# Optimization experiments

Hardware: AMD Instinct MI355X
Metric: run time of the kernel (lower is better)

The kernel has to match this reference:

```python
import jax, jax.numpy as jnp
import numpy as np

N, A, C = 4, 8732, 81
SCALE_XY, SCALE_WH = 0.1, 0.2   # dboxes.scale_xy / scale_wh; Loss uses reciprocals
LAM, W_IOU = 1.0, 0.01
EPS_IOU = float(np.finfo(float).eps)


def setup_inputs() -> dict:
    key = jax.random.key(0)
    ks = jax.random.split(key, 8)
    ploc = jax.random.normal(ks[0], (N, 4, A), dtype=jnp.float32) * 0.5
    plabel = jax.random.normal(ks[1], (N, C, A), dtype=jnp.float32)
    # ground-truth loc in xywh with strictly positive wh (loc_vec takes a log)
    gxy = jax.random.uniform(ks[2], (N, 2, A), dtype=jnp.float32)
    gwh = jax.random.uniform(ks[3], (N, 2, A), dtype=jnp.float32) * 0.4 + 0.05
    gloc = jnp.concatenate([gxy, gwh], axis=1)
    lab = jax.random.randint(ks[4], (N, A), 1, C)
    keep = jax.random.uniform(ks[5], (N, A)) < 0.02
    glabel = jnp.where(keep, lab, 0).astype(jnp.int32)
    # default boxes in xywh, shape [1, 4, A]
    dxy = jax.random.uniform(ks[6], (1, 2, A), dtype=jnp.float32)
    dwh = jax.random.uniform(ks[7], (1, 2, A), dtype=jnp.float32) * 0.45 + 0.05
    dboxes = jnp.concatenate([dxy, dwh], axis=1)
    return {"ploc": ploc, "plabel": plabel, "gloc": gloc, "glabel": glabel, "dboxes": dboxes}


def _decode_ltrb(loc, dboxes):
    """scale_back_batch: encoded [N,4,A] + dboxes xywh [1,4,A] -> ltrb [N,A,4]."""
    b = jnp.transpose(loc, (0, 2, 1))      # [N, A, 4]
    d = jnp.transpose(dboxes, (0, 2, 1))   # [1, A, 4]
    xy = SCALE_XY * b[..., :2] * d[..., 2:] + d[..., :2]
    wh = jnp.exp(SCALE_WH * b[..., 2:]) * d[..., 2:]
    return jnp.concatenate([xy - 0.5 * wh, xy + 0.5 * wh], axis=-1)


def _iou_sum(p, g):
    """p, g: [A,4] ltrb -> per-anchor sum over all g boxes of IoU(p_i, g_k)."""
    area_p = (p[:, 2] - p[:, 0]) * (p[:, 3] - p[:, 1])
    area_g = (g[:, 2] - g[:, 0]) * (g[:, 3] - g[:, 1])
    iw = jnp.maximum(jnp.minimum(p[:, None, 2], g[None, :, 2]) - jnp.maximum(p[:, None, 0], g[None, :, 0]), 0.0)
    ih = jnp.maximum(jnp.minimum(p[:, None, 3], g[None, :, 3]) - jnp.maximum(p[:, None, 1], g[None, :, 1]), 0.0)
    inter = iw * ih                                      # [A, A]
    ua = jnp.maximum(area_p[:, None] + area_g[None, :] - inter, EPS_IOU)
    return (inter / ua).sum(axis=1)                      # [A]


def _forward(ploc, plabel, gloc, glabel, dboxes):
    mask = glabel > 0                                    # [N, A]
    pos_num = mask.sum(axis=1)                           # [N]

    # loc_vec: encode ground truth against default boxes
    dxy, dwh = dboxes[:, :2, :], dboxes[:, 2:, :]
    gxy_t = (1.0 / SCALE_XY) * (gloc[:, :2, :] - dxy) / dwh
    gwh_t = (1.0 / SCALE_WH) * jnp.log(gloc[:, 2:, :] / dwh)
    vec_gd = jnp.concatenate([gxy_t, gwh_t], axis=1)     # [N, 4, A]

    # SmoothL1 (beta=1), summed over coord dim
    diff = ploc - vec_gd
    ad = jnp.abs(diff)
    sl1 = jnp.where(ad < 1.0, 0.5 * diff * diff, ad - 0.5).sum(axis=1)  # [N, A]

    # per-anchor cross entropy
    logp = jax.nn.log_softmax(plabel, axis=1)            # [N, C, A]
    con = -jnp.take_along_axis(logp, glabel[:, None, :], axis=1)[:, 0, :]  # [N, A]

    # weighted-IoU reweighting (weights are detached in the original)
    p_ltrb = _decode_ltrb(ploc, dboxes)                  # [N, A, 4]
    g_ltrb = _decode_ltrb(gloc, dboxes)
    iou_s = jax.vmap(_iou_sum)(p_ltrb, g_ltrb)           # [N, A]
    valid = (p_ltrb[..., 0] < p_ltrb[..., 2]) & (p_ltrb[..., 1] < p_ltrb[..., 3])
    weights = jnp.where(valid, W_IOU * iou_s ** LAM, 0.0)
    weights = jax.lax.stop_gradient(weights)
    sl1 = (sl1 / (sl1 + weights)) * sl1

    sl1_pos = (mask.astype(sl1.dtype) * sl1).sum(axis=1)  # [N]

    # hard negative mining: double argsort for ranks
    con_neg = jnp.where(mask, 0.0, con)
    con_idx = jnp.argsort(-con_neg, axis=1)
    con_rank = jnp.argsort(con_idx, axis=1)
    neg_num = jnp.minimum(3 * pos_num, A)[:, None]
    neg_mask = con_rank < neg_num
    closs = (con * (mask.astype(con.dtype) + neg_mask.astype(con.dtype))).sum(axis=1)

    total = sl1_pos + closs
    num_mask = (pos_num > 0).astype(total.dtype)
    pn = jnp.maximum(pos_num.astype(total.dtype), 1e-6)
    return (total * num_mask / pn).mean()


def reference(ploc, plabel, gloc, glabel, dboxes):
    return _forward(ploc, plabel, gloc, glabel, dboxes)
```

## Files before the change

### kernel.cpp

```cpp
#include <hip/hip_runtime.h>
#include <math.h>

#define A_N 8732
#define NAT (4 * A_N)
#define BATCH 4
#define CLS 81
#define TILE 256
#define NBINS 2048
#define PLB 128

__device__ __forceinline__ float sl1f(float d) {
    float ad = fabsf(d);
    return ad < 1.0f ? 0.5f * d * d : ad - 0.5f;
}
__device__ __forceinline__ unsigned umap(float v) {
    return __float_as_uint(v) | 0x80000000u;
}

__device__ void suffix_find(const int* lcnt, const float* lsum, int k, int tid,
                            int* ic, float* fsum,
                            int* o_b, int* o_krem, float* o_sumA)
{
    int base = tid * 8;
    int cs = 0; float ss = 0.0f;
    #pragma unroll
    for (int j = 0; j < 8; j++) { cs += lcnt[base + j]; ss += lsum[base + j]; }
    ic[tid] = cs; fsum[tid] = ss;
    __syncthreads();
    for (int off = 1; off < TILE; off <<= 1) {
        int v = ic[tid]; float f = fsum[tid];
        int v2 = 0; float f2 = 0.0f;
        if (tid + off < TILE) { v2 = ic[tid + off]; f2 = fsum[tid + off]; }
        __syncthreads();
        ic[tid] = v + v2; fsum[tid] = f + f2;
        __syncthreads();
    }
    int run = ic[tid] - cs;
    float runs = fsum[tid] - ss;
    for (int j = 7; j >= 0; j--) {
        int b = base + j; int c = lcnt[b];
        if (run < k && run + c >= k) { *o_b = b; *o_krem = k - run; *o_sumA = runs; }
        run += c; runs += lsum[b];
    }
    __syncthreads();
}

__global__ __launch_bounds__(TILE) void prep_kernel(
    const float* __restrict__ ploc, const float* __restrict__ plabel,
    const float* __restrict__ gloc, const int* __restrict__ glabel,
    const float* __restrict__ dboxes,
    float4* __restrict__ pbox, float4* __restrict__ gbox,
    float* __restrict__ sl1raw, float* __restrict__ conneg,
    int* __restrict__ poslist, int* __restrict__ posnum,
    float* __restrict__ sums, int* __restrict__ h1cnt, float* __restrict__ h1sum)
{
    __shared__ int   lcnt[NBINS];
    __shared__ float lsum[NBINS];
    const int tid = threadIdx.x;
    const int a = blockIdx.x * TILE + tid;
    const int n = blockIdx.y;
    for (int b = tid; b < NBINS; b += TILE) { lcnt[b] = 0; lsum[b] = 0.0f; }
    __syncthreads();

    if (a < A_N) {
        const float* pb = plabel + (size_t)n * CLS * A_N + a;
        float se = 0.0f;
        #pragma unroll 27
        for (int c = 0; c < CLS; c++) se += expf(pb[(size_t)c * A_N]);
        int lab = glabel[n * A_N + a];
        float xg = pb[(size_t)lab * A_N];
        float cv = logf(se) - xg;
        bool msk = lab > 0;
        float cng = msk ? 0.0f : cv;
        conneg[n * A_N + a] = cng;
        if (msk) {
            int pos = atomicAdd(&posnum[n], 1);
            poslist[n * A_N + pos] = a;
            atomicAdd(&sums[n], cv);
        }
        int d = (umap(cng) >> 20) & (NBINS - 1);
        atomicAdd(&lcnt[d], 1);
        atomicAdd(&lsum[d], cng);

        float d0 = dboxes[0*A_N+a], d1 = dboxes[1*A_N+a], d2 = dboxes[2*A_N+a], d3 = dboxes[3*A_N+a];
        const float* pl = ploc + (size_t)n * 4 * A_N;
        const float* gl = gloc + (size_t)n * 4 * A_N;
        float p0 = pl[0*A_N+a], p1 = pl[1*A_N+a], p2 = pl[2*A_N+a], p3 = pl[3*A_N+a];
        float g0 = gl[0*A_N+a], g1 = gl[1*A_N+a], g2 = gl[2*A_N+a], g3 = gl[3*A_N+a];

        float v0 = 10.0f * (g0 - d0) / d2;
        float v1 = 10.0f * (g1 - d1) / d3;
        float v2 = 5.0f * logf(g2 / d2);
        float v3 = 5.0f * logf(g3 / d3);
        sl1raw[n * A_N + a] = sl1f(p0-v0) + sl1f(p1-v1) + sl1f(p2-v2) + sl1f(p3-v3);

        float cx = 0.1f*p0*d2 + d0, cy = 0.1f*p1*d3 + d1;
        float cw = expf(0.2f*p2)*d2, ch = expf(0.2f*p3)*d3;
        pbox[(size_t)n*A_N + a] = make_float4(cx-0.5f*cw, cy-0.5f*ch, cx+0.5f*cw, cy+0.5f*ch);
        float ex = 0.1f*g0*d2 + d0, ey = 0.1f*g1*d3 + d1;
        float ew = expf(0.2f*g2)*d2, eh = expf(0.2f*g3)*d3;
        gbox[(size_t)n*A_N + a] = make_float4(ex-0.5f*ew, ey-0.5f*eh, ex+0.5f*ew, ey+0.5f*eh);
    }
    __syncthreads();
    for (int b = tid; b < NBINS; b += TILE)
        if (lcnt[b]) { atomicAdd(&h1cnt[n * NBINS + b], lcnt[b]); atomicAdd(&h1sum[n * NBINS + b], lsum[b]); }
}

__global__ __launch_bounds__(TILE) void tail_kernel(
    const float4* __restrict__ pbox, const float4* __restrict__ gbox,
    const float* __restrict__ sl1raw, const float* __restrict__ conneg,
    const int* __restrict__ poslist, const int* __restrict__ posnum,
    const float* __restrict__ sums,
    const int* __restrict__ h1cnt, const float* __restrict__ h1sum,
    float* __restrict__ out)
{
    __shared__ int   lcnt[NBINS];
    __shared__ float lsum[NBINS];
    __shared__ int   ic[TILE];
    __shared__ float fs_[TILE];
    __shared__ int sb1, skrem1, sb2, skrem2;
    __shared__ float ssA1, ssA2;
    __shared__ float r4[4];
    const int n = blockIdx.y, tid = threadIdx.x;
    const int np = posnum[n];
    if (np <= 0) return;
    const float inv = 1.0f / ((float)np * (float)BATCH);

    if (blockIdx.x < PLB) {
        for (int p = blockIdx.x; p < np; p += PLB) {
            int a = poslist[n * A_N + p];
            float4 b = pbox[(size_t)n * A_N + a];
            float ap = (b.z - b.x) * (b.w - b.y);
            float acc = 0.0f;
            for (int k = tid; k < A_N; k += TILE) {
                float4 g = gbox[(size_t)n * A_N + k];
                float iw = fmaxf(fminf(b.z, g.z) - fmaxf(b.x, g.x), 0.0f);
                float ih = fmaxf(fminf(b.w, g.w) - fmaxf(b.y, g.y), 0.0f);
                float inter = iw * ih;
                float ua = ap + (g.z - g.x) * (g.w - g.y) - inter;
                acc += inter * __builtin_amdgcn_rcpf(ua);
            }
            #pragma unroll
            for (int off = 32; off > 0; off >>= 1) acc += __shfl_down(acc, off);
            if ((tid & 63) == 0) r4[tid >> 6] = acc;
            __syncthreads();
            if (tid == 0) {
                float iou = r4[0] + r4[1] + r4[2] + r4[3];
                bool valid = (b.x < b.z) && (b.y < b.w);
                float w = valid ? 0.01f * iou : 0.0f;
                float s = sl1raw[n * A_N + a];
                atomicAdd(out, (s / (s + w) * s) * inv);
            }
            __syncthreads();
        }
    } else {
        int k = min(3 * np, A_N);
        for (int b = tid; b < NBINS; b += TILE) { lcnt[b] = h1cnt[n * NBINS + b]; lsum[b] = h1sum[n * NBINS + b]; }
        __syncthreads();
        suffix_find(lcnt, lsum, k, tid, ic, fs_, &sb1, &skrem1, &ssA1);
        int b1 = sb1;
        __syncthreads();

        for (int b = tid; b < NBINS; b += TILE) { lcnt[b] = 0; lsum[b] = 0.0f; }
        __syncthreads();
        for (int i = tid; i < A_N; i += TILE) {
            float v = conneg[n * A_N + i];
            unsigned u = umap(v);
            if ((int)((u >> 20) & (NBINS - 1)) == b1) {
                int d = (u >> 9) & (NBINS - 1);
                atomicAdd(&lcnt[d], 1);
                atomicAdd(&lsum[d], v);
            }
        }
        __syncthreads();
        suffix_find(lcnt, lsum, skrem1, tid, ic, fs_, &sb2, &skrem2, &ssA2);

        if (tid == 0) {
            unsigned ubin = 0x80000000u | ((unsigned)sb1 << 20) | ((unsigned)sb2 << 9) | 256u;
            float tval = __uint_as_float(ubin & 0x7fffffffu);
            float closs_neg = ssA1 + ssA2 + (float)skrem2 * tval;
            atomicAdd(out, (sums[n] + closs_neg) * inv);
        }
    }
}

extern "C" void kernel_launch(void* const* d_in, const int* in_sizes, int n_in,
                              void* d_out, int out_size, void* d_ws, size_t ws_size,
                              hipStream_t stream) {
    const float* ploc   = (const float*)d_in[0];
    const float* plabel = (const float*)d_in[1];
    const float* gloc   = (const float*)d_in[2];
    const int*   glabel = (const int*)d_in[3];
    const float* dboxes = (const float*)d_in[4];
    float* out = (float*)d_out;

    int*    h1cnt  = (int*)d_ws;
    float*  h1sum  = (float*)(h1cnt + BATCH * NBINS);
    int*    posnum = (int*)(h1sum + BATCH * NBINS);
    float*  sums   = (float*)(posnum + BATCH);
    float4* pbox   = (float4*)(sums + BATCH);
    float4* gbox   = pbox + NAT;
    float*  sl1raw = (float*)(gbox + NAT);
    float*  conneg = sl1raw + NAT;
    int*    poslist = (int*)(conneg + NAT);

    const size_t zbytes = (size_t)(2 * BATCH * NBINS + 2 * BATCH) * 4;

    hipMemsetAsync(d_ws, 0, zbytes, stream);
    hipMemsetAsync(d_out, 0, sizeof(float), stream);
    prep_kernel<<<dim3((A_N + TILE - 1) / TILE, BATCH), TILE, 0, stream>>>(
        ploc, plabel, gloc, glabel, dboxes,
        pbox, gbox, sl1raw, conneg, poslist, posnum, sums, h1cnt, h1sum);
    tail_kernel<<<dim3(PLB + 1, BATCH), TILE, 0, stream>>>(
        pbox, gbox, sl1raw, conneg, poslist, posnum, sums, h1cnt, h1sum, out);
}
```

Measured before the change: 111.4 us.

## Replace global atomics and workspace memset with per-block compaction and tail-side histogram

The prep kernel no longer uses global atomics for the positive count, the positive list or the loss sum. Each block now compacts its positives with a wave ballot and writes a per-block count and sum. The first-level histogram of negative confidences moves from prep (shared plus global atomics) into the single mining block of the tail kernel, so the workspace memset disappears. In exchange, the mining block must rescan conneg serially, and every tail block rebuilds a prefix over the per-block counts.

```diff
diff --git a/kernel.cpp b/kernel.cpp
--- a/kernel.cpp
+++ b/kernel.cpp
@@ -6,6 +6,7 @@
 #define BATCH 4
 #define CLS 81
 #define TILE 256
+#define ABLK 35
 #define NBINS 2048
 #define PLB 128
 
@@ -51,17 +52,19 @@
     const float* __restrict__ dboxes,
     float4* __restrict__ pbox, float4* __restrict__ gbox,
     float* __restrict__ sl1raw, float* __restrict__ conneg,
-    int* __restrict__ poslist, int* __restrict__ posnum,
-    float* __restrict__ sums, int* __restrict__ h1cnt, float* __restrict__ h1sum)
+    int* __restrict__ poslist,
+    int* __restrict__ poscnt,
+    float* __restrict__ consum)
 {
-    __shared__ int   lcnt[NBINS];
-    __shared__ float lsum[NBINS];
+    __shared__ int   wcnt[4];
+    __shared__ float wsum[4];
     const int tid = threadIdx.x;
-    const int a = blockIdx.x * TILE + tid;
+    const int blk = blockIdx.x;
+    const int a = blk * TILE + tid;
     const int n = blockIdx.y;
-    for (int b = tid; b < NBINS; b += TILE) { lcnt[b] = 0; lsum[b] = 0.0f; }
-    __syncthreads();
-
+
+    bool msk = false;
+    float cv = 0.0f;
     if (a < A_N) {
         const float* pb = plabel + (size_t)n * CLS * A_N + a;
         float se = 0.0f;
@@ -69,18 +72,9 @@
         for (int c = 0; c < CLS; c++) se += expf(pb[(size_t)c * A_N]);
         int lab = glabel[n * A_N + a];
         float xg = pb[(size_t)lab * A_N];
-        float cv = logf(se) - xg;
-        bool msk = lab > 0;
-        float cng = msk ? 0.0f : cv;
-        conneg[n * A_N + a] = cng;
-        if (msk) {
-            int pos = atomicAdd(&posnum[n], 1);
-            poslist[n * A_N + pos] = a;
-            atomicAdd(&sums[n], cv);
-        }
-        int d = (umap(cng) >> 20) & (NBINS - 1);
-        atomicAdd(&lcnt[d], 1);
-        atomicAdd(&lsum[d], cng);
+        cv = logf(se) - xg;
+        msk = lab > 0;
+        conneg[n * A_N + a] = msk ? 0.0f : cv;
 
         float d0 = dboxes[0*A_N+a], d1 = dboxes[1*A_N+a], d2 = dboxes[2*A_N+a], d3 = dboxes[3*A_N+a];
         const float* pl = ploc + (size_t)n * 4 * A_N;
@@ -101,34 +95,53 @@
         float ew = expf(0.2f*g2)*d2, eh = expf(0.2f*g3)*d3;
         gbox[(size_t)n*A_N + a] = make_float4(ex-0.5f*ew, ey-0.5f*eh, ex+0.5f*ew, ey+0.5f*eh);
     }
-    __syncthreads();
-    for (int b = tid; b < NBINS; b += TILE)
-        if (lcnt[b]) { atomicAdd(&h1cnt[n * NBINS + b], lcnt[b]); atomicAdd(&h1sum[n * NBINS + b], lsum[b]); }
+
+    unsigned long long bal = __ballot(msk);
+    int wid = tid >> 6, lane = tid & 63;
+    float wv = msk ? cv : 0.0f;
+    #pragma unroll
+    for (int off = 32; off > 0; off >>= 1) wv += __shfl_down(wv, off);
+    if (lane == 0) { wcnt[wid] = __popcll(bal); wsum[wid] = wv; }
+    __syncthreads();
+    if (msk) {
+        int base = 0;
+        for (int w = 0; w < wid; w++) base += wcnt[w];
+        int off = base + (int)__popcll(bal & ((1ULL << lane) - 1ULL));
+        poslist[(n * ABLK + blk) * TILE + off] = a;
+    }
+    if (tid == 0) {
+        poscnt[n * ABLK + blk] = wcnt[0] + wcnt[1] + wcnt[2] + wcnt[3];
+        consum[n * ABLK + blk] = wsum[0] + wsum[1] + wsum[2] + wsum[3];
+    }
 }
 
 __global__ __launch_bounds__(TILE) void tail_kernel(
     const float4* __restrict__ pbox, const float4* __restrict__ gbox,
     const float* __restrict__ sl1raw, const float* __restrict__ conneg,
-    const int* __restrict__ poslist, const int* __restrict__ posnum,
-    const float* __restrict__ sums,
-    const int* __restrict__ h1cnt, const float* __restrict__ h1sum,
+    const int* __restrict__ poslist, const int* __restrict__ poscnt,
+    const float* __restrict__ consum,
     float* __restrict__ out)
 {
-    __shared__ int   lcnt[NBINS];
-    __shared__ float lsum[NBINS];
-    __shared__ int   ic[TILE];
-    __shared__ float fs_[TILE];
-    __shared__ int sb1, skrem1, sb2, skrem2;
-    __shared__ float ssA1, ssA2;
+    __shared__ int   spre[ABLK + 1];
     __shared__ float r4[4];
     const int n = blockIdx.y, tid = threadIdx.x;
-    const int np = posnum[n];
+
+    if (tid == 0) {
+        int run = 0;
+        #pragma unroll
+        for (int s = 0; s < ABLK; s++) { spre[s] = run; run += poscnt[n * ABLK + s]; }
+        spre[ABLK] = run;
+    }
+    __syncthreads();
+    const int np = spre[ABLK];
     if (np <= 0) return;
     const float inv = 1.0f / ((float)np * (float)BATCH);
 
     if (blockIdx.x < PLB) {
         for (int p = blockIdx.x; p < np; p += PLB) {
-            int a = poslist[n * A_N + p];
+            int s = 0;
+            while (spre[s + 1] <= p) s++;
+            int a = poslist[(n * ABLK + s) * TILE + (p - spre[s])];
             float4 b = pbox[(size_t)n * A_N + a];
             float ap = (b.z - b.x) * (b.w - b.y);
             float acc = 0.0f;
@@ -148,14 +161,28 @@
                 float iou = r4[0] + r4[1] + r4[2] + r4[3];
                 bool valid = (b.x < b.z) && (b.y < b.w);
                 float w = valid ? 0.01f * iou : 0.0f;
-                float s = sl1raw[n * A_N + a];
-                atomicAdd(out, (s / (s + w) * s) * inv);
+                float sv = sl1raw[n * A_N + a];
+                atomicAdd(out, (sv / (sv + w) * sv) * inv);
             }
             __syncthreads();
         }
     } else {
+        __shared__ int   lcnt[NBINS];
+        __shared__ float lsum[NBINS];
+        __shared__ int   ic[TILE];
+        __shared__ float fs_[TILE];
+        __shared__ int sb1, skrem1, sb2, skrem2;
+        __shared__ float ssA1, ssA2;
         int k = min(3 * np, A_N);
-        for (int b = tid; b < NBINS; b += TILE) { lcnt[b] = h1cnt[n * NBINS + b]; lsum[b] = h1sum[n * NBINS + b]; }
+
+        for (int b = tid; b < NBINS; b += TILE) { lcnt[b] = 0; lsum[b] = 0.0f; }
+        __syncthreads();
+        for (int i = tid; i < A_N; i += TILE) {
+            float v = conneg[n * A_N + i];
+            int d = (umap(v) >> 20) & (NBINS - 1);
+            atomicAdd(&lcnt[d], 1);
+            atomicAdd(&lsum[d], v);
+        }
         __syncthreads();
         suffix_find(lcnt, lsum, k, tid, ic, fs_, &sb1, &skrem1, &ssA1);
         int b1 = sb1;
@@ -176,10 +203,13 @@
         suffix_find(lcnt, lsum, skrem1, tid, ic, fs_, &sb2, &skrem2, &ssA2);
 
         if (tid == 0) {
+            float conpos = 0.0f;
+            #pragma unroll
+            for (int s = 0; s < ABLK; s++) conpos += consum[n * ABLK + s];
             unsigned ubin = 0x80000000u | ((unsigned)sb1 << 20) | ((unsigned)sb2 << 9) | 256u;
             float tval = __uint_as_float(ubin & 0x7fffffffu);
             float closs_neg = ssA1 + ssA2 + (float)skrem2 * tval;
-            atomicAdd(out, (sums[n] + closs_neg) * inv);
+            atomicAdd(out, (conpos + closs_neg) * inv);
         }
     }
 }
@@ -194,23 +224,18 @@
     const float* dboxes = (const float*)d_in[4];
     float* out = (float*)d_out;
 
-    int*    h1cnt  = (int*)d_ws;
-    float*  h1sum  = (float*)(h1cnt + BATCH * NBINS);
-    int*    posnum = (int*)(h1sum + BATCH * NBINS);
-    float*  sums   = (float*)(posnum + BATCH);
-    float4* pbox   = (float4*)(sums + BATCH);
-    float4* gbox   = pbox + NAT;
-    float*  sl1raw = (float*)(gbox + NAT);
-    float*  conneg = sl1raw + NAT;
+    float4* pbox    = (float4*)d_ws;
+    float4* gbox    = pbox + NAT;
+    float*  sl1raw  = (float*)(gbox + NAT);
+    float*  conneg  = sl1raw + NAT;
     int*    poslist = (int*)(conneg + NAT);
-
-    const size_t zbytes = (size_t)(2 * BATCH * NBINS + 2 * BATCH) * 4;
-
-    hipMemsetAsync(d_ws, 0, zbytes, stream);
+    int*    poscnt  = poslist + BATCH * ABLK * TILE;
+    float*  consum  = (float*)(poscnt + BATCH * ABLK);
+
     hipMemsetAsync(d_out, 0, sizeof(float), stream);
-    prep_kernel<<<dim3((A_N + TILE - 1) / TILE, BATCH), TILE, 0, stream>>>(
+    prep_kernel<<<dim3(ABLK, BATCH), TILE, 0, stream>>>(
         ploc, plabel, gloc, glabel, dboxes,
-        pbox, gbox, sl1raw, conneg, poslist, posnum, sums, h1cnt, h1sum);
+        pbox, gbox, sl1raw, conneg, poslist, poscnt, consum);
     tail_kernel<<<dim3(PLB + 1, BATCH), TILE, 0, stream>>>(
-        pbox, gbox, sl1raw, conneg, poslist, posnum, sums, h1cnt, h1sum, out);
-}
+        pbox, gbox, sl1raw, conneg, poslist, poscnt, consum, out);
+}
```

After: 103.5 us, median of 2. -7.1%, faster.
